# Optimization experiments

Measured on AMD Instinct MI355X. Metric: run time of the kernel, lower is better.

Reference implementation:

```python
import jax, jax.numpy as jnp
import numpy as np

EMBED_DIM = 2048
HEAD_DIM = 128
B, T = 4, 2048


def setup_inputs() -> dict:
    key = jax.random.key(0)
    k1, k2, k3, k4 = jax.random.split(key, 4)
    x_in = jax.random.normal(k1, (B, T, EMBED_DIM), dtype=jnp.float32)
    scale = 1.0 / np.sqrt(EMBED_DIM)
    Wq = jax.random.normal(k2, (EMBED_DIM, HEAD_DIM), dtype=jnp.float32) * scale
    Wk = jax.random.normal(k3, (EMBED_DIM, HEAD_DIM), dtype=jnp.float32) * scale
    Wv = jax.random.normal(k4, (EMBED_DIM, HEAD_DIM), dtype=jnp.float32) * scale
    return {"x_in": x_in, "Wq": Wq, "Wk": Wk, "Wv": Wv}


def reference(x_in, Wq, Wk, Wv):
    # x_in: [B, T, E]; projections (Linear, no bias)
    q = jnp.einsum('bte,ed->btd', x_in, Wq)  # [B,T,D]
    k = jnp.einsum('bte,ed->btd', x_in, Wk)
    v = jnp.einsum('bte,ed->btd', x_in, Wv)
    t = x_in.shape[1]
    d = Wq.shape[1]
    s = jnp.einsum('btd,bsd->bts', q, k) / jnp.sqrt(jnp.asarray(d, q.dtype))  # [B,Tq,Tk]
    # causal mask: positions with tril==0 (k index > q index) -> -inf
    causal = jnp.tril(jnp.ones((t, t), dtype=bool))
    s = jnp.where(causal, s, -jnp.inf)
    # NOTE: original module applies softmax over dim=1 (query axis), faithfully reproduced
    a = jax.nn.softmax(s, axis=1)
    z = jnp.einsum('bts,bsd->btd', a, v)  # [B,T,D]
    return z
```

## Files before the change

### kernel.cpp

```cpp
#include <hip/hip_runtime.h>

typedef _Float16 f16x8 __attribute__((ext_vector_type(8)));
typedef _Float16 f16x4 __attribute__((ext_vector_type(4)));
typedef float f32x4 __attribute__((ext_vector_type(4)));

#define T_DIM 2048
#define E_DIM 2048
#define D_DIM 128
#define NB 4
#define KSP_P 4
#define KCH_P 512
#define KSP_A 8
#define KCH_A 256
#define NCH2 32
#define ST_LD 136

__device__ __forceinline__ void gll16(const void* g, void* l) {
  __builtin_amdgcn_global_load_lds(
      (const __attribute__((address_space(1))) unsigned int*)g,
      (__attribute__((address_space(3))) unsigned int*)l, 16, 0, 0);
}

__device__ __forceinline__ void merge_stat(float& m, float& l, float pm, float pl) {
  if (pm != -__builtin_inff()) {
    float nm = fmaxf(m, pm);
    l = l * __expf(m - nm) + pl * __expf(pm - nm);
    m = nm;
  }
}


__global__ void cvt_w(const float* __restrict__ Wq, const float* __restrict__ Wk,
                      const float* __restrict__ Wv, _Float16* __restrict__ WhT) {
  int idx = blockIdx.x * 256 + threadIdx.x;
  int w = blockIdx.y;
  const float* W = (w == 0) ? Wq : ((w == 1) ? Wk : Wv);
  int e = idx & (E_DIM - 1), d = idx >> 11;
  WhT[(size_t)w * (D_DIM * E_DIM) + idx] = (_Float16)W[e * D_DIM + d];
}


__global__ __launch_bounds__(256) void proj_gemm(
    const float* __restrict__ x, const _Float16* __restrict__ WhT,
    _Float16* __restrict__ Ph) {
  __shared__ _Float16 Asw[2][128 * 32];
  __shared__ _Float16 Bsw[2][128 * 32];
  const int tid = threadIdx.x, w = tid >> 6, lane = tid & 63;
  const int wr = w >> 1, wc = w & 1, quad = lane >> 4, l16 = lane & 15;
  const int t0 = blockIdx.x * 128;
  const int wsel = blockIdx.y, ks = blockIdx.z;
  const _Float16* B = WhT + (size_t)wsel * (D_DIM * E_DIM);
  const int arow0 = tid >> 2, aseg = tid & 3;
  const int brow = tid >> 2, bseg = tid & 3;
  const int kstart = ks * KCH_P, kend = kstart + KCH_P;

  f32x4 pa[2][2];

#define LOADA(kk)                                                         \
  do {                                                                    \
    _Pragma("unroll") for (int p = 0; p < 2; ++p) {                       \
      int row = p * 64 + arow0;                                           \
      const float* xp = x + (size_t)(t0 + row) * E_DIM + (kk) + aseg * 8; \
      pa[p][0] = *(const f32x4*)xp;                                       \
      pa[p][1] = *(const f32x4*)(xp + 4);                                 \
    }                                                                     \
  } while (0)

#define WRITEA(bufi)                                                      \
  do {                                                                    \
    _Pragma("unroll") for (int p = 0; p < 2; ++p) {                       \
      int row = p * 64 + arow0;                                           \
      f16x8 o;                                                            \
      _Pragma("unroll") for (int e = 0; e < 4; ++e) {                     \
        o[e] = (_Float16)pa[p][0][e];                                     \
        o[e + 4] = (_Float16)pa[p][1][e];                                 \
      }                                                                   \
      int sg = aseg ^ ((row >> 1) & 3);                                   \
      *(f16x8*)(Asw[bufi] + row * 32 + sg * 8) = o;                       \
    }                                                                     \
  } while (0)

#define DMAB(bufi, kk)                                                    \
  do {                                                                    \
    _Pragma("unroll") for (int p = 0; p < 2; ++p) {                       \
      int row = p * 64 + brow;                                            \
      int gseg = bseg ^ ((row >> 1) & 3);                                 \
      gll16(B + (size_t)row * E_DIM + (kk) + gseg * 8,                    \
            Bsw[bufi] + row * 32 + bseg * 8);                             \
    }                                                                     \
  } while (0)

  LOADA(kstart);
  WRITEA(0);
  DMAB(0, kstart);
  LOADA(kstart + 32);
  f32x4 acc[4][4] = {};
  int buf = 0;
  for (int k0 = kstart; k0 < kend; k0 += 32) {
    __syncthreads();
    if (k0 + 32 < kend) {
      WRITEA(buf ^ 1);
      DMAB(buf ^ 1, k0 + 32);
      if (k0 + 64 < kend) LOADA(k0 + 64);
    }
    f16x8 af[4], bf[4];
#pragma unroll
    for (int i = 0; i < 4; ++i) {
      int row = wr * 64 + i * 16 + l16;
      int sg = quad ^ ((row >> 1) & 3);
      af[i] = *(const f16x8*)(Asw[buf] + row * 32 + sg * 8);
    }
#pragma unroll
    for (int j = 0; j < 4; ++j) {
      int row = wc * 64 + j * 16 + l16;
      int sg = quad ^ ((row >> 1) & 3);
      bf[j] = *(const f16x8*)(Bsw[buf] + row * 32 + sg * 8);
    }
#pragma unroll
    for (int i = 0; i < 4; ++i)
#pragma unroll
      for (int j = 0; j < 4; ++j)
        acc[i][j] = __builtin_amdgcn_mfma_f32_16x16x32_f16(af[i], bf[j], acc[i][j], 0, 0, 0);
    buf ^= 1;
  }
#undef LOADA
#undef WRITEA
#undef DMAB
  _Float16* P = Ph + ((size_t)(ks * 3 + wsel) << 20);
  if (wsel < 2) {
#pragma unroll
    for (int i = 0; i < 4; ++i)
#pragma unroll
      for (int j = 0; j < 4; ++j) {
        int n = wc * 64 + j * 16 + l16;
#pragma unroll
        for (int r = 0; r < 4; ++r) {
          int t = t0 + wr * 64 + i * 16 + quad * 4 + r;
          P[(size_t)t * D_DIM + n] = (_Float16)acc[i][j][r];
        }
      }
  } else {
#pragma unroll
    for (int i = 0; i < 4; ++i)
#pragma unroll
      for (int j = 0; j < 4; ++j) {
        int n = wc * 64 + j * 16 + l16;
        int t = t0 + wr * 64 + i * 16 + quad * 4;
        f16x4 o;
#pragma unroll
        for (int r = 0; r < 4; ++r) o[r] = (_Float16)acc[i][j][r];
        *(f16x4*)(P + ((size_t)(t >> 11) * D_DIM + n) * T_DIM + (t & (T_DIM - 1))) = o;
      }
  }
}


__global__ void proj_reduce(const _Float16* __restrict__ Ph, _Float16* __restrict__ Qh,
                            _Float16* __restrict__ Kh, _Float16* __restrict__ VT) {
  size_t u = ((size_t)blockIdx.x * 256 + threadIdx.x) * 8;
  int mat = (int)(u >> 20);
  size_t rem = u & ((1u << 20) - 1);
  float s[8] = {};
#pragma unroll
  for (int ks = 0; ks < KSP_P; ++ks) {
    f16x8 p = *(const f16x8*)(Ph + ((size_t)(ks * 3 + mat) << 20) + rem);
#pragma unroll
    for (int e = 0; e < 8; ++e) s[e] += (float)p[e];
  }
  f16x8 o;
#pragma unroll
  for (int e = 0; e < 8; ++e) o[e] = (_Float16)s[e];
  _Float16* dst = (mat == 0) ? Qh : ((mat == 1) ? Kh : VT);
  *(f16x8*)(dst + rem) = o;
}


__global__ __launch_bounds__(256) void s_gemm(const _Float16* __restrict__ Qh,
                                              const _Float16* __restrict__ Kh,
                                              _Float16* __restrict__ S,
                                              float* __restrict__ Pm,
                                              float* __restrict__ Pl) {
  int idx = blockIdx.x;
  int xt = (int)((sqrtf(8.f * idx + 1.f) - 1.f) * 0.5f);
  while ((xt + 1) * (xt + 2) / 2 <= idx) ++xt;
  while (xt * (xt + 1) / 2 > idx) --xt;
  int yt = idx - xt * (xt + 1) / 2;
  __shared__ __align__(16) char smem[128 * ST_LD * 2];
  _Float16* Bs = (_Float16*)smem;
  _Float16* St = (_Float16*)smem;
  const int tid = threadIdx.x, w = tid >> 6, lane = tid & 63;
  const int wr = w >> 1, wc = w & 1, quad = lane >> 4, l16 = lane & 15;
  const int t0 = xt * 128, s0 = yt * 128, b = blockIdx.y;
  const _Float16* A = Qh + (size_t)b * T_DIM * D_DIM;
  const _Float16* B = Kh + (size_t)b * T_DIM * D_DIM;
  const int srow = lane >> 2;
  const int swz = ((lane & 3) ^ ((srow >> 1) & 3)) * 8;
#pragma unroll
  for (int kq = 0; kq < 4; ++kq)
#pragma unroll
    for (int q = 0; q < 2; ++q) {
      int rbase = w * 32 + q * 16;
      gll16(B + (size_t)(s0 + rbase + srow) * D_DIM + kq * 32 + swz,
            Bs + kq * 4096 + rbase * 32);
    }
  __syncthreads();
  f32x4 acc[4][4] = {};
  const int bsg = (quad ^ ((l16 >> 1) & 3)) * 8;
#pragma unroll
  for (int kq = 0; kq < 4; ++kq) {
    f16x8 af[4], bf[4];
#pragma unroll
    for (int i = 0; i < 4; ++i)
      af[i] = *(const f16x8*)(A + (size_t)(t0 + wr * 64 + i * 16 + l16) * D_DIM +
                              kq * 32 + quad * 8);
#pragma unroll
    for (int j = 0; j < 4; ++j)
      bf[j] = *(const f16x8*)(Bs + kq * 4096 + (wc * 64 + j * 16 + l16) * 32 + bsg);
#pragma unroll
    for (int i = 0; i < 4; ++i)
#pragma unroll
      for (int j = 0; j < 4; ++j)
        acc[i][j] = __builtin_amdgcn_mfma_f32_16x16x32_f16(af[i], bf[j], acc[i][j], 0, 0, 0);
  }
  const float scale = 0.08838834764831845f;
  const float NEG = -__builtin_inff();
  __syncthreads();
#pragma unroll
  for (int j = 0; j < 4; ++j) {
    const int s = s0 + wc * 64 + j * 16 + l16;
    const int sloc = wc * 64 + j * 16 + l16;
    float m = NEG;
#pragma unroll
    for (int i = 0; i < 4; ++i)
#pragma unroll
      for (int r = 0; r < 4; ++r) {
        int tloc = wr * 64 + i * 16 + quad * 4 + r;
        float v = (s > t0 + tloc) ? NEG : acc[i][j][r] * scale;
        St[tloc * ST_LD + sloc] = (_Float16)v;
        m = fmaxf(m, v);
      }
    float l = 0.f;
    if (m != NEG) {
#pragma unroll
      for (int i = 0; i < 4; ++i)
#pragma unroll
        for (int r = 0; r < 4; ++r) {
          int tloc = wr * 64 + i * 16 + quad * 4 + r;
          float v = (s > t0 + tloc) ? NEG : acc[i][j][r] * scale;
          l += __expf(v - m);
        }
    }
#pragma unroll
    for (int d = 16; d <= 32; d <<= 1) {
      float pm = __shfl_xor(m, d, 64);
      float pl = __shfl_xor(l, d, 64);
      merge_stat(m, l, pm, pl);
    }
    if (quad == 0) {
      int c = 2 * xt + wr;
      Pm[((size_t)c * NB + b) * T_DIM + s] = m;
      Pl[((size_t)c * NB + b) * T_DIM + s] = l;
    }
  }
  __syncthreads();
  _Float16* Sb = S + (size_t)b * T_DIM * T_DIM;
  const int rr = tid >> 1, hh = tid & 1;
#pragma unroll
  for (int e = 0; e < 8; ++e) {
    f16x8 v = *(const f16x8*)(St + rr * ST_LD + hh * 64 + e * 8);
    *(f16x8*)(Sb + (size_t)(t0 + rr) * T_DIM + s0 + hh * 64 + e * 8) = v;
  }
}


__global__ __launch_bounds__(256) void av_gemm(const _Float16* __restrict__ S,
                                               const _Float16* __restrict__ VT,
                                               const float* __restrict__ Pm,
                                               const float* __restrict__ Pl,
                                               float* __restrict__ Zp) {
  const int t0 = blockIdx.x * 128, b = blockIdx.y, ks = blockIdx.z;
  const int Kmax = t0 + 128;
  const int Kstart = ks * KCH_A;
  if (Kstart >= Kmax) return;
  const int Kend = (Kstart + KCH_A < Kmax) ? (Kstart + KCH_A) : Kmax;
  __shared__ _Float16 As[128 * 32];
  __shared__ _Float16 Bs[128 * 32];
  __shared__ float Ms[KCH_A];
  __shared__ float Ls[KCH_A];
  const int tid = threadIdx.x, w = tid >> 6, lane = tid & 63;
  const int wr = w >> 1, wc = w & 1, quad = lane >> 4, l16 = lane & 15;
  const _Float16* Sb = S + (size_t)b * T_DIM * T_DIM;
  const _Float16* Vb = VT + (size_t)b * D_DIM * T_DIM;
  {
    int s = Kstart + tid;
    float m = -__builtin_inff(), l = 0.f;
    for (int ch = s >> 6; ch < NCH2; ++ch) {
      size_t pidx = ((size_t)ch * NB + b) * T_DIM + s;
      merge_stat(m, l, Pm[pidx], Pl[pidx]);
    }
    Ms[tid] = m;
    Ls[tid] = 1.f / l;
  }
  const int srow = lane >> 2, scol = (lane & 3) * 8;
  f32x4 acc[4][4] = {};
  for (int k0 = Kstart; k0 < Kend; k0 += 32) {
    __syncthreads();
#pragma unroll
    for (int q = 0; q < 2; ++q) {
      int u = q * 256 + tid;
      int row = u >> 2, c8 = (u & 3) * 8;
      int sc = k0 + c8;
      f16x8 v = *(const f16x8*)(Sb + (size_t)(t0 + row) * T_DIM + sc);
      f16x8 o;
#pragma unroll
      for (int e = 0; e < 8; ++e) {
        int li = sc + e - Kstart;
        float a = __expf((float)v[e] - Ms[li]) * Ls[li];
        o[e] = (_Float16)a;
      }
      *(f16x8*)(As + row * 32 + c8) = o;
      int rbase = w * 32 + q * 16;
      gll16(Vb + (size_t)(rbase + srow) * T_DIM + k0 + scol, Bs + rbase * 32);
    }
    __syncthreads();
    f16x8 af[4], bf[4];
#pragma unroll
    for (int i = 0; i < 4; ++i)
      af[i] = *(const f16x8*)(As + (wr * 64 + i * 16 + l16) * 32 + quad * 8);
#pragma unroll
    for (int j = 0; j < 4; ++j)
      bf[j] = *(const f16x8*)(Bs + (wc * 64 + j * 16 + l16) * 32 + quad * 8);
#pragma unroll
    for (int i = 0; i < 4; ++i)
#pragma unroll
      for (int j = 0; j < 4; ++j)
        acc[i][j] = __builtin_amdgcn_mfma_f32_16x16x32_f16(af[i], bf[j], acc[i][j], 0, 0, 0);
  }
  float* Zb = Zp + ((size_t)ks * NB + b) * T_DIM * D_DIM;
#pragma unroll
  for (int i = 0; i < 4; ++i)
#pragma unroll
    for (int j = 0; j < 4; ++j) {
      int n = wc * 64 + j * 16 + l16;
#pragma unroll
      for (int r = 0; r < 4; ++r) {
        int t = t0 + wr * 64 + i * 16 + quad * 4 + r;
        Zb[(size_t)t * D_DIM + n] = acc[i][j][r];
      }
    }
}


__global__ void z_reduce(const float* __restrict__ Zp, float* __restrict__ Z) {
  size_t flat = ((size_t)blockIdx.x * 256 + threadIdx.x) * 4;
  int t = (int)((flat >> 7) & (T_DIM - 1));
  int ns = ((t >> 7) + 2) >> 1;
  f32x4 s = {};
  for (int ks = 0; ks < ns; ++ks) {
    f32x4 p = *(const f32x4*)(Zp + ((size_t)ks * NB * T_DIM * D_DIM) + flat);
    s += p;
  }
  *(f32x4*)(Z + flat) = s;
}


extern "C" void kernel_launch(void* const* d_in, const int* in_sizes, int n_in,
                              void* d_out, int out_size, void* d_ws, size_t ws_size,
                              hipStream_t stream) {
  const float* x = (const float*)d_in[0];
  const float* Wq = (const float*)d_in[1];
  const float* Wk = (const float*)d_in[2];
  const float* Wv = (const float*)d_in[3];
  char* ws = (char*)d_ws;
  float* Zp = (float*)(ws);
  _Float16* WhT = (_Float16*)(ws + 33554432);
  _Float16* Qh = (_Float16*)(ws + 35127296);
  _Float16* Kh = (_Float16*)(ws + 37224448);
  _Float16* VT = (_Float16*)(ws + 39321600);
  _Float16* S = (_Float16*)(ws + 41418752);
  _Float16* Ph = (_Float16*)(ws + 41418752);
  float* Pm = (float*)(ws + 75038720);
  float* Pl = (float*)(ws + 76087296);
  float* Z = (float*)d_out;

  cvt_w<<<dim3(1024, 3), 256, 0, stream>>>(Wq, Wk, Wv, WhT);
  proj_gemm<<<dim3(64, 3, KSP_P), 256, 0, stream>>>(x, WhT, Ph);
  proj_reduce<<<1536, 256, 0, stream>>>(Ph, Qh, Kh, VT);
  s_gemm<<<dim3(136, 4), 256, 0, stream>>>(Qh, Kh, S, Pm, Pl);
  av_gemm<<<dim3(16, 4, KSP_A), 256, 0, stream>>>(S, VT, Pm, Pl, Zp);
  z_reduce<<<1024, 256, 0, stream>>>(Zp, Z);
}
```

Measured before the change: 186.3 us.

## Fuse Q/K/V projection tiles per block and precombine softmax column stats

The projection GEMM now has each block compute a 64-column slice of all three of Q, K and V. Each x tile is then converted to fp16 and staged in LDS once per block for all three weight matrices, not once per weight, which cuts redundant x reads and conversions by a third. A new comb_stats kernel merges the per-chunk max/sum softmax statistics once per column. av_gemm then simply loads the final M and 1/L instead of every block re-merging up to 32 partials. The costs are an extra kernel launch, more accumulators in proj_gemm (which may lower occupancy), and fewer projection blocks (512 vs 768).

```diff
diff --git a/kernel.cpp b/kernel.cpp
--- a/kernel.cpp
+++ b/kernel.cpp
@@ -44,12 +44,11 @@
     const float* __restrict__ x, const _Float16* __restrict__ WhT,
     _Float16* __restrict__ Ph) {
   __shared__ _Float16 Asw[2][128 * 32];
-  __shared__ _Float16 Bsw[2][128 * 32];
+  __shared__ _Float16 Bsw[2][3][64 * 32];
   const int tid = threadIdx.x, w = tid >> 6, lane = tid & 63;
   const int wr = w >> 1, wc = w & 1, quad = lane >> 4, l16 = lane & 15;
   const int t0 = blockIdx.x * 128;
-  const int wsel = blockIdx.y, ks = blockIdx.z;
-  const _Float16* B = WhT + (size_t)wsel * (D_DIM * E_DIM);
+  const int dh = blockIdx.y, ks = blockIdx.z;
   const int arow0 = tid >> 2, aseg = tid & 3;
   const int brow = tid >> 2, bseg = tid & 3;
   const int kstart = ks * KCH_P, kend = kstart + KCH_P;
@@ -82,11 +81,11 @@
 
 #define DMAB(bufi, kk)                                                    \
   do {                                                                    \
-    _Pragma("unroll") for (int p = 0; p < 2; ++p) {                       \
-      int row = p * 64 + brow;                                            \
-      int gseg = bseg ^ ((row >> 1) & 3);                                 \
-      gll16(B + (size_t)row * E_DIM + (kk) + gseg * 8,                    \
-            Bsw[bufi] + row * 32 + bseg * 8);                             \
+    _Pragma("unroll") for (int m = 0; m < 3; ++m) {                       \
+      int gseg = bseg ^ ((brow >> 1) & 3);                                \
+      gll16(WhT + (size_t)m * (D_DIM * E_DIM) +                           \
+                (size_t)(dh * 64 + brow) * E_DIM + (kk) + gseg * 8,       \
+            Bsw[bufi][m] + brow * 32 + bseg * 8);                         \
     }                                                                     \
   } while (0)
 
@@ -94,7 +93,7 @@
   WRITEA(0);
   DMAB(0, kstart);
   LOADA(kstart + 32);
-  f32x4 acc[4][4] = {};
+  f32x4 acc[3][4][2] = {};
   int buf = 0;
   for (int k0 = kstart; k0 < kend; k0 += 32) {
     __syncthreads();
@@ -103,7 +102,7 @@
       DMAB(buf ^ 1, k0 + 32);
       if (k0 + 64 < kend) LOADA(k0 + 64);
     }
-    f16x8 af[4], bf[4];
+    f16x8 af[4];
 #pragma unroll
     for (int i = 0; i < 4; ++i) {
       int row = wr * 64 + i * 16 + l16;
@@ -111,46 +110,54 @@
       af[i] = *(const f16x8*)(Asw[buf] + row * 32 + sg * 8);
     }
 #pragma unroll
-    for (int j = 0; j < 4; ++j) {
-      int row = wc * 64 + j * 16 + l16;
-      int sg = quad ^ ((row >> 1) & 3);
-      bf[j] = *(const f16x8*)(Bsw[buf] + row * 32 + sg * 8);
-    }
-#pragma unroll
-    for (int i = 0; i < 4; ++i)
-#pragma unroll
-      for (int j = 0; j < 4; ++j)
-        acc[i][j] = __builtin_amdgcn_mfma_f32_16x16x32_f16(af[i], bf[j], acc[i][j], 0, 0, 0);
+    for (int m = 0; m < 3; ++m) {
+      f16x8 bf[2];
+#pragma unroll
+      for (int j = 0; j < 2; ++j) {
+        int row = wc * 32 + j * 16 + l16;
+        int sg = quad ^ ((row >> 1) & 3);
+        bf[j] = *(const f16x8*)(Bsw[buf][m] + row * 32 + sg * 8);
+      }
+#pragma unroll
+      for (int i = 0; i < 4; ++i)
+#pragma unroll
+        for (int j = 0; j < 2; ++j)
+          acc[m][i][j] =
+              __builtin_amdgcn_mfma_f32_16x16x32_f16(af[i], bf[j], acc[m][i][j], 0, 0, 0);
+    }
     buf ^= 1;
   }
 #undef LOADA
 #undef WRITEA
 #undef DMAB
-  _Float16* P = Ph + ((size_t)(ks * 3 + wsel) << 20);
-  if (wsel < 2) {
-#pragma unroll
-    for (int i = 0; i < 4; ++i)
-#pragma unroll
-      for (int j = 0; j < 4; ++j) {
-        int n = wc * 64 + j * 16 + l16;
-#pragma unroll
-        for (int r = 0; r < 4; ++r) {
-          int t = t0 + wr * 64 + i * 16 + quad * 4 + r;
-          P[(size_t)t * D_DIM + n] = (_Float16)acc[i][j][r];
+#pragma unroll
+  for (int m = 0; m < 3; ++m) {
+    _Float16* P = Ph + ((size_t)(ks * 3 + m) << 20);
+    if (m < 2) {
+#pragma unroll
+      for (int i = 0; i < 4; ++i)
+#pragma unroll
+        for (int j = 0; j < 2; ++j) {
+          int n = dh * 64 + wc * 32 + j * 16 + l16;
+#pragma unroll
+          for (int r = 0; r < 4; ++r) {
+            int t = t0 + wr * 64 + i * 16 + quad * 4 + r;
+            P[(size_t)t * D_DIM + n] = (_Float16)acc[m][i][j][r];
+          }
         }
-      }
-  } else {
-#pragma unroll
-    for (int i = 0; i < 4; ++i)
-#pragma unroll
-      for (int j = 0; j < 4; ++j) {
-        int n = wc * 64 + j * 16 + l16;
-        int t = t0 + wr * 64 + i * 16 + quad * 4;
-        f16x4 o;
-#pragma unroll
-        for (int r = 0; r < 4; ++r) o[r] = (_Float16)acc[i][j][r];
-        *(f16x4*)(P + ((size_t)(t >> 11) * D_DIM + n) * T_DIM + (t & (T_DIM - 1))) = o;
-      }
+    } else {
+#pragma unroll
+      for (int i = 0; i < 4; ++i)
+#pragma unroll
+        for (int j = 0; j < 2; ++j) {
+          int n = dh * 64 + wc * 32 + j * 16 + l16;
+          int t = t0 + wr * 64 + i * 16 + quad * 4;
+          f16x4 o;
+#pragma unroll
+          for (int r = 0; r < 4; ++r) o[r] = (_Float16)acc[m][i][j][r];
+          *(f16x4*)(P + ((size_t)(t >> 11) * D_DIM + n) * T_DIM + (t & (T_DIM - 1))) = o;
+        }
+    }
   }
 }
 
@@ -273,10 +280,42 @@
 }
 
 
+__global__ __launch_bounds__(256) void comb_stats(const float* __restrict__ Pm,
+                                                  const float* __restrict__ Pl,
+                                                  float* __restrict__ M,
+                                                  float* __restrict__ L) {
+  __shared__ float sM[8][32];
+  __shared__ float sL[8][32];
+  const int g = threadIdx.x >> 5, sl = threadIdx.x & 31;
+  const int c = blockIdx.x * 32 + sl;
+  const int b = c >> 11, s = c & (T_DIM - 1);
+  float m = -__builtin_inff(), l = 0.f;
+#pragma unroll
+  for (int k = 0; k < NCH2 / 8; ++k) {
+    int ch = g * (NCH2 / 8) + k;
+    if (ch >= (s >> 6)) {
+      size_t idx = ((size_t)ch * NB + b) * T_DIM + s;
+      merge_stat(m, l, Pm[idx], Pl[idx]);
+    }
+  }
+  sM[g][sl] = m;
+  sL[g][sl] = l;
+  __syncthreads();
+  if (threadIdx.x < 32) {
+    const int c2 = blockIdx.x * 32 + threadIdx.x;
+    float fm = -__builtin_inff(), fl = 0.f;
+#pragma unroll
+    for (int gg = 0; gg < 8; ++gg) merge_stat(fm, fl, sM[gg][threadIdx.x], sL[gg][threadIdx.x]);
+    M[c2] = fm;
+    L[c2] = 1.f / fl;
+  }
+}
+
+
 __global__ __launch_bounds__(256) void av_gemm(const _Float16* __restrict__ S,
                                                const _Float16* __restrict__ VT,
-                                               const float* __restrict__ Pm,
-                                               const float* __restrict__ Pl,
+                                               const float* __restrict__ M,
+                                               const float* __restrict__ L,
                                                float* __restrict__ Zp) {
   const int t0 = blockIdx.x * 128, b = blockIdx.y, ks = blockIdx.z;
   const int Kmax = t0 + 128;
@@ -291,15 +330,9 @@
   const int wr = w >> 1, wc = w & 1, quad = lane >> 4, l16 = lane & 15;
   const _Float16* Sb = S + (size_t)b * T_DIM * T_DIM;
   const _Float16* Vb = VT + (size_t)b * D_DIM * T_DIM;
-  {
-    int s = Kstart + tid;
-    float m = -__builtin_inff(), l = 0.f;
-    for (int ch = s >> 6; ch < NCH2; ++ch) {
-      size_t pidx = ((size_t)ch * NB + b) * T_DIM + s;
-      merge_stat(m, l, Pm[pidx], Pl[pidx]);
-    }
-    Ms[tid] = m;
-    Ls[tid] = 1.f / l;
+  for (int i = tid; i < Kend - Kstart; i += 256) {
+    Ms[i] = M[b * T_DIM + Kstart + i];
+    Ls[i] = L[b * T_DIM + Kstart + i];
   }
   const int srow = lane >> 2, scol = (lane & 3) * 8;
   f32x4 acc[4][4] = {};
@@ -379,14 +412,17 @@
   _Float16* VT = (_Float16*)(ws + 39321600);
   _Float16* S = (_Float16*)(ws + 41418752);
   _Float16* Ph = (_Float16*)(ws + 41418752);
+  float* M = (float*)(ws + 74973184);
+  float* L = (float*)(ws + 75005952);
   float* Pm = (float*)(ws + 75038720);
   float* Pl = (float*)(ws + 76087296);
   float* Z = (float*)d_out;
 
   cvt_w<<<dim3(1024, 3), 256, 0, stream>>>(Wq, Wk, Wv, WhT);
-  proj_gemm<<<dim3(64, 3, KSP_P), 256, 0, stream>>>(x, WhT, Ph);
+  proj_gemm<<<dim3(64, 2, KSP_P), 256, 0, stream>>>(x, WhT, Ph);
   proj_reduce<<<1536, 256, 0, stream>>>(Ph, Qh, Kh, VT);
   s_gemm<<<dim3(136, 4), 256, 0, stream>>>(Qh, Kh, S, Pm, Pl);
-  av_gemm<<<dim3(16, 4, KSP_A), 256, 0, stream>>>(S, VT, Pm, Pl, Zp);
+  comb_stats<<<256, 256, 0, stream>>>(Pm, Pl, M, L);
+  av_gemm<<<dim3(16, 4, KSP_A), 256, 0, stream>>>(S, VT, M, L, Zp);
   z_reduce<<<1024, 256, 0, stream>>>(Zp, Z);
 }
```

New measurement: 176.7 us. 5.1% less time.
